# Kernel optimization log

Measured on AMD Instinct MI355X. Metric: run time of the kernel, lower is better.

## Reference

```python
import jax, jax.numpy as jnp
import numpy as np

B, S, D, DFF, H, V, L = 2, 1024, 1024, 4096, 16, 32000, 8
DH = D // H
EPS = 1e-5

def _pe():
    pos = np.arange(S, dtype=np.float32)[:, None]
    div = np.exp(np.arange(0, D, 2, dtype=np.float32) * (-np.log(10000.0) / D))
    pe = np.zeros((S, D), dtype=np.float32)
    pe[:, 0::2] = np.sin(pos * div)
    pe[:, 1::2] = np.cos(pos * div)
    return jnp.asarray(pe)

PE = _pe()

def _ln(h, g, b):
    m = jnp.mean(h, axis=-1, keepdims=True)
    v = jnp.mean((h - m) ** 2, axis=-1, keepdims=True)
    return (h - m) * jax.lax.rsqrt(v + EPS) * g + b

def setup_inputs():
    key = jax.random.key(0)
    k = jax.random.split(key, 16)
    sc = 0.02
    return {
        'x': jax.random.randint(k[0], (B, S), 0, V),
        'mask': jnp.tril(jnp.ones((1, 1, S, S), dtype=bool)),
        'emb': jax.random.normal(k[1], (V, D)) * sc,
        'Wq': jax.random.normal(k[2], (L, D, D)) * sc,
        'Wk': jax.random.normal(k[3], (L, D, D)) * sc,
        'Wv': jax.random.normal(k[4], (L, D, D)) * sc,
        'Wo': jax.random.normal(k[5], (L, D, D)) * sc,
        'ln1_g': jnp.ones((L, D)), 'ln1_b': jnp.zeros((L, D)),
        'ln2_g': jnp.ones((L, D)), 'ln2_b': jnp.zeros((L, D)),
        'W1': jax.random.normal(k[6], (L, D, DFF)) * sc,
        'b1': jnp.zeros((L, DFF)),
        'W2': jax.random.normal(k[7], (L, DFF, D)) * sc,
        'b2': jnp.zeros((L, D)),
        'lnf_g': jnp.ones((D,)), 'lnf_b': jnp.zeros((D,)),
        'projW': jax.random.normal(k[8], (D, V)) * sc,
        'projb': jnp.zeros((V,)),
    }

def reference(x, mask, emb, Wq, Wk, Wv, Wo, ln1_g, ln1_b, ln2_g, ln2_b,
              W1, b1, W2, b2, lnf_g, lnf_b, projW, projb):
    # embedding * sqrt(D) + positional encoding
    h = emb[x] * jnp.sqrt(jnp.float32(D)) + PE[None, :, :]
    scale = 1.0 / jnp.sqrt(jnp.float32(DH))
    for i in range(L):
        # --- self-attention sublayer (pre-LN residual) ---
        a_in = _ln(h, ln1_g[i], ln1_b[i])
        q = (a_in @ Wq[i]).reshape(B, S, H, DH)
        kk = (a_in @ Wk[i]).reshape(B, S, H, DH)
        v = (a_in @ Wv[i]).reshape(B, S, H, DH)
        scores = jnp.einsum('bqhd,bkhd->bhqk', q, kk) * scale
        scores = jnp.where(mask, scores, -1e9)
        attn = jax.nn.softmax(scores, axis=-1)
        o = jnp.einsum('bhqk,bkhd->bqhd', attn, v).reshape(B, S, D)
        h = h + o @ Wo[i]
        # --- feed-forward sublayer ---
        f_in = _ln(h, ln2_g[i], ln2_b[i])
        h = h + (jax.nn.relu(f_in @ W1[i] + b1[i]) @ W2[i] + b2[i])
    h = _ln(h, lnf_g, lnf_b)
    return h @ projW + projb
```

## Files before the change

### kernel.cpp

```cpp
#include <hip/hip_runtime.h>

typedef __bf16 bf16;
typedef __bf16 bf16x4 __attribute__((ext_vector_type(4)));
typedef __bf16 bf16x8 __attribute__((ext_vector_type(8)));
typedef float f32x4 __attribute__((ext_vector_type(4)));
typedef short short4v __attribute__((ext_vector_type(4)));

__device__ __forceinline__ short f2bs(float x) {
  bf16 hv = (bf16)x;
  return __builtin_bit_cast(short, hv);
}

__device__ __forceinline__ void gl_lds16(const void* g, void* l) {
  __builtin_amdgcn_global_load_lds(
      (const __attribute__((address_space(1))) unsigned int*)g,
      (__attribute__((address_space(3))) unsigned int*)l, 16, 0, 0);
}

__global__ __launch_bounds__(256) void wt_k(const float* __restrict__ in,
    bf16* __restrict__ out, int K, int N, long in_ls, long out_ls)
{
  __shared__ float t[64][33];
  const int z = blockIdx.z;
  const float* ip = in + (size_t)z * in_ls;
  bf16* op = out + (size_t)z * out_ls;
  const int n0 = blockIdx.x * 32, k0 = blockIdx.y * 64;
  const int tid = threadIdx.x;
  const int kr = tid >> 3, nc = (tid & 7) * 4;
#pragma unroll
  for (int hh = 0; hh < 2; ++hh) {
    float4 v = *(const float4*)(ip + (size_t)(k0 + kr + hh * 32) * N + n0 + nc);
    t[kr + hh * 32][nc]     = v.x;
    t[kr + hh * 32][nc + 1] = v.y;
    t[kr + hh * 32][nc + 2] = v.z;
    t[kr + hh * 32][nc + 3] = v.w;
  }
  __syncthreads();
  const int nr = tid >> 3, kc = (tid & 7) * 8;
  bf16x8 o;
#pragma unroll
  for (int j = 0; j < 8; ++j) o[j] = (bf16)t[kc + j][nr];
  *(bf16x8*)(op + (size_t)(n0 + nr) * K + k0 + kc) = o;
}

__global__ __launch_bounds__(256) void wt4_k(const float* __restrict__ Wq,
    const float* __restrict__ Wk, const float* __restrict__ Wv,
    const float* __restrict__ Wo, bf16* __restrict__ Bqkv,
    bf16* __restrict__ Bo)
{
  __shared__ float t[64][33];
  const int z = blockIdx.z;
  const int which = z >> 3, layer = z & 7;
  const long M1 = 1024 * 1024, M3 = 3 * M1;
  const float* ip = (which == 0 ? Wq : which == 1 ? Wk : which == 2 ? Wv : Wo)
                    + (size_t)layer * M1;
  bf16* op = (which < 3) ? (Bqkv + (size_t)layer * M3 + (size_t)which * M1)
                         : (Bo + (size_t)layer * M1);
  const int n0 = blockIdx.x * 32, k0 = blockIdx.y * 64;
  const int tid = threadIdx.x;
  const int kr = tid >> 3, nc = (tid & 7) * 4;
#pragma unroll
  for (int hh = 0; hh < 2; ++hh) {
    float4 v = *(const float4*)(ip + (size_t)(k0 + kr + hh * 32) * 1024 + n0 + nc);
    t[kr + hh * 32][nc]     = v.x;
    t[kr + hh * 32][nc + 1] = v.y;
    t[kr + hh * 32][nc + 2] = v.z;
    t[kr + hh * 32][nc + 3] = v.w;
  }
  __syncthreads();
  const int nr = tid >> 3, kc = (tid & 7) * 8;
  bf16x8 o;
#pragma unroll
  for (int j = 0; j < 8; ++j) o[j] = (bf16)t[kc + j][nr];
  *(bf16x8*)(op + (size_t)(n0 + nr) * 1024 + k0 + kc) = o;
}

__global__ __launch_bounds__(256) void embed_k(const int* __restrict__ x,
    const float* __restrict__ emb, float* __restrict__ h)
{
  const int m = blockIdx.x, t = threadIdx.x;
  const int s = m & 1023;
  const int tok = x[m];
  const int d0 = t * 4;
  float4 e = *(const float4*)(emb + (size_t)tok * 1024 + d0);
  const float* ep = &e.x;
  float r[4];
#pragma unroll
  for (int j = 0; j < 4; ++j) {
    int d = d0 + j;
    float freq = expf((float)(d & ~1) * (-9.2103403719761836f / 1024.f));
    float ang = (float)s * freq;
    float pe = (d & 1) ? cosf(ang) : sinf(ang);
    r[j] = ep[j] * 32.f + pe;
  }
  *(float4*)(h + (size_t)m * 1024 + d0) = make_float4(r[0], r[1], r[2], r[3]);
}

__global__ __launch_bounds__(256) void ln_k(const float* __restrict__ h,
    const float* __restrict__ g, const float* __restrict__ b,
    bf16* __restrict__ out)
{
  const int row = blockIdx.x, t = threadIdx.x;
  const float* hr = h + (size_t)row * 1024;
  float4 x = *(const float4*)(hr + t * 4);
  float s  = x.x + x.y + x.z + x.w;
  float ss = x.x * x.x + x.y * x.y + x.z * x.z + x.w * x.w;
#pragma unroll
  for (int off = 32; off >= 1; off >>= 1) {
    s  += __shfl_down(s, off);
    ss += __shfl_down(ss, off);
  }
  __shared__ float sb[4], ssb[4];
  if ((t & 63) == 0) { sb[t >> 6] = s; ssb[t >> 6] = ss; }
  __syncthreads();
  s  = sb[0] + sb[1] + sb[2] + sb[3];
  ss = ssb[0] + ssb[1] + ssb[2] + ssb[3];
  const float mean = s * (1.f / 1024.f);
  const float var  = ss * (1.f / 1024.f) - mean * mean;
  const float rstd = rsqrtf(var + 1e-5f);
  const float* xp = &x.x;
#pragma unroll
  for (int j = 0; j < 4; ++j) {
    int d = t * 4 + j;
    out[(size_t)row * 1024 + d] = (bf16)((xp[j] - mean) * rstd * g[d] + b[d]);
  }
}

__global__ __launch_bounds__(1024) void gemm256_k(
    const bf16* __restrict__ A, const bf16* __restrict__ Bt,
    const float* __restrict__ bias, float* __restrict__ C,
    int M, int N, int K)
{
  __shared__ __align__(16) bf16 As[2][256 * 64];
  __shared__ __align__(16) bf16 Bs[2][256 * 64];

  const int nwg = gridDim.x;
  const int orig = blockIdx.x;
  const int q8 = nwg >> 3, r8 = nwg & 7;
  const int xcd = orig & 7, loc = orig >> 3;
  const int wg = (xcd < r8 ? xcd * (q8 + 1) : r8 * (q8 + 1) + (xcd - r8) * q8) + loc;
  const int nrowt = M >> 8;
  const int rowt = wg & (nrowt - 1);
  const int colt = wg / nrowt;
  const int m0 = rowt * 256;
  const int n0 = colt * 256;
  const int nt = K >> 6;

  const int tid = threadIdx.x;
  const int lane = tid & 63;
  const int wbase = tid & ~63;
  const int wid = tid >> 6;
  const int wm = wid >> 2, wn = wid & 3;
  const int qr = lane & 15, grp = lane >> 4;

  f32x4 acc[4][4];
#pragma unroll
  for (int i = 0; i < 4; ++i)
#pragma unroll
    for (int j = 0; j < 4; ++j) acc[i][j] = (f32x4){0.f, 0.f, 0.f, 0.f};

  auto stage = [&](int bufi, int kt) {
#pragma unroll
    for (int it = 0; it < 2; ++it) {
      const int idx = it * 1024 + tid;
      const int row = idx >> 3, c = idx & 7;
      const int bo = (c * 16) ^ ((row & 7) << 4);
      gl_lds16((const char*)(A + (size_t)(m0 + row) * K + kt) + bo,
               (char*)&As[bufi][0] + (size_t)(it * 1024 + wbase) * 16);
    }
#pragma unroll
    for (int it = 0; it < 2; ++it) {
      const int idx = it * 1024 + tid;
      const int row = idx >> 3, c = idx & 7;
      const int bo = (c * 16) ^ ((row & 7) << 4);
      gl_lds16((const char*)(Bt + (size_t)(n0 + row) * K + kt) + bo,
               (char*)&Bs[bufi][0] + (size_t)(it * 1024 + wbase) * 16);
    }
  };

  stage(0, 0);
  for (int t = 0; t < nt; ++t) {
    const int cur = t & 1;
    if (t + 1 < nt) {
      stage(cur ^ 1, (t + 1) * 64);
      asm volatile("s_waitcnt vmcnt(4)" ::: "memory");
    } else {
      asm volatile("s_waitcnt vmcnt(0)" ::: "memory");
    }
    __builtin_amdgcn_s_barrier();
    asm volatile("" ::: "memory");
#pragma unroll
    for (int ks = 0; ks < 2; ++ks) {
      bf16x8 af[4], bfr[4];
#pragma unroll
      for (int mi = 0; mi < 4; ++mi) {
        const int arow = wm * 64 + mi * 16 + qr;
        const int ab = arow * 128 + ((grp * 16 + ks * 64) ^ ((arow & 7) << 4));
        af[mi] = *(const bf16x8*)((const char*)&As[cur][0] + ab);
      }
#pragma unroll
      for (int ni = 0; ni < 4; ++ni) {
        const int brow = wn * 64 + ni * 16 + qr;
        const int bb = brow * 128 + ((grp * 16 + ks * 64) ^ ((brow & 7) << 4));
        bfr[ni] = *(const bf16x8*)((const char*)&Bs[cur][0] + bb);
      }
      __builtin_amdgcn_s_setprio(1);
#pragma unroll
      for (int mi = 0; mi < 4; ++mi)
#pragma unroll
        for (int ni = 0; ni < 4; ++ni)
          acc[mi][ni] = __builtin_amdgcn_mfma_f32_16x16x32_bf16(
              bfr[ni], af[mi], acc[mi][ni], 0, 0, 0);
      __builtin_amdgcn_s_setprio(0);
    }
    __builtin_amdgcn_s_barrier();
    asm volatile("" ::: "memory");
  }

#pragma unroll
  for (int mi = 0; mi < 4; ++mi) {
    const int rowg = m0 + wm * 64 + mi * 16 + qr;
#pragma unroll
    for (int ni = 0; ni < 4; ++ni) {
      const int colg = n0 + wn * 64 + ni * 16 + grp * 4;
      float4 bv = *(const float4*)(bias + colg);
      float4 o;
      o.x = acc[mi][ni][0] + bv.x;
      o.y = acc[mi][ni][1] + bv.y;
      o.z = acc[mi][ni][2] + bv.z;
      o.w = acc[mi][ni][3] + bv.w;
      *(float4*)(C + (size_t)rowg * N + colg) = o;
    }
  }
}

template<int MODE, int NSPLIT>
__global__ __launch_bounds__(512) void gemm8_k(
    const bf16* __restrict__ A, const bf16* __restrict__ Bt,
    const float* __restrict__ bias, void* __restrict__ Cout,
    float* __restrict__ Hacc, bf16* __restrict__ Vt,
    int M, int N, int K)
{
  __shared__ __align__(16) bf16 As[2][128 * 64];
  __shared__ __align__(16) bf16 Bs[2][128 * 64];

  const int nwg = gridDim.x;
  const int orig = blockIdx.x;
  const int q8 = nwg >> 3, r8 = nwg & 7;
  const int xcd = orig & 7, loc = orig >> 3;
  const int wg = (xcd < r8 ? xcd * (q8 + 1) : r8 * (q8 + 1) + (xcd - r8) * q8) + loc;
  const int nrowt = M >> 7;
  const int ntiles = nrowt * (N >> 7);
  const int split = (NSPLIT > 1) ? (wg / ntiles) : 0;
  const int tile  = (NSPLIT > 1) ? (wg % ntiles) : wg;
  const int rowt = tile & (nrowt - 1);
  const int colt = tile / nrowt;
  const int m0 = rowt * 128;
  const int n0 = colt * 128;
  const int Ks = K / NSPLIT;
  const int k_begin = split * Ks;
  const int nt = Ks >> 6;

  const int tid = threadIdx.x;
  const int lane = tid & 63;
  const int wbase = tid & ~63;
  const int wid = tid >> 6;
  const int wm = wid >> 2;
  const int wn = wid & 3;
  const int qr = lane & 15, grp = lane >> 4;

  f32x4 acc[4][2];
#pragma unroll
  for (int i = 0; i < 4; ++i)
#pragma unroll
    for (int j = 0; j < 2; ++j) acc[i][j] = (f32x4){0.f, 0.f, 0.f, 0.f};

  auto stage = [&](int bufi, int kt) {
#pragma unroll
    for (int it = 0; it < 2; ++it) {
      const int idx = it * 512 + tid;
      const int row = idx >> 3, c = idx & 7;
      const int bo = (c * 16) ^ ((row & 7) << 4);
      gl_lds16((const char*)(A + (size_t)(m0 + row) * K + kt) + bo,
               (char*)&As[bufi][0] + (size_t)(it * 512 + wbase) * 16);
    }
#pragma unroll
    for (int it = 0; it < 2; ++it) {
      const int idx = it * 512 + tid;
      const int row = idx >> 3, c = idx & 7;
      const int bo = (c * 16) ^ ((row & 7) << 4);
      gl_lds16((const char*)(Bt + (size_t)(n0 + row) * K + kt) + bo,
               (char*)&Bs[bufi][0] + (size_t)(it * 512 + wbase) * 16);
    }
  };

  stage(0, k_begin);
  for (int t = 0; t < nt; ++t) {
    const int cur = t & 1;
    if (t + 1 < nt) {
      stage(cur ^ 1, k_begin + (t + 1) * 64);
      asm volatile("s_waitcnt vmcnt(4)" ::: "memory");
    } else {
      asm volatile("s_waitcnt vmcnt(0)" ::: "memory");
    }
    __builtin_amdgcn_s_barrier();
    asm volatile("" ::: "memory");
#pragma unroll
    for (int ks = 0; ks < 2; ++ks) {
      bf16x8 af[4], bfr[2];
#pragma unroll
      for (int mi = 0; mi < 4; ++mi) {
        const int arow = wm * 64 + mi * 16 + qr;
        const int ab = arow * 128 + ((grp * 16 + ks * 64) ^ ((arow & 7) << 4));
        af[mi] = *(const bf16x8*)((const char*)&As[cur][0] + ab);
      }
#pragma unroll
      for (int ni = 0; ni < 2; ++ni) {
        const int brow = wn * 32 + ni * 16 + qr;
        const int bb = brow * 128 + ((grp * 16 + ks * 64) ^ ((brow & 7) << 4));
        bfr[ni] = *(const bf16x8*)((const char*)&Bs[cur][0] + bb);
      }
      __builtin_amdgcn_s_setprio(1);
#pragma unroll
      for (int mi = 0; mi < 4; ++mi)
#pragma unroll
        for (int ni = 0; ni < 2; ++ni)
          acc[mi][ni] = __builtin_amdgcn_mfma_f32_16x16x32_bf16(
              af[mi], bfr[ni], acc[mi][ni], 0, 0, 0);
      __builtin_amdgcn_s_setprio(0);
    }
    __builtin_amdgcn_s_barrier();
    asm volatile("" ::: "memory");
  }

  const int sel = (MODE == 5) ? (n0 >> 10) : 0;
#pragma unroll
  for (int ni = 0; ni < 2; ++ni) {
    const int coln = wn * 32 + ni * 16 + qr;
    const int colg = n0 + coln;
    float bv = 0.f;
    if (MODE == 1) bv = bias[colg];
    if (MODE == 3 && split == 0) bv = bias[colg];
#pragma unroll
    for (int mi = 0; mi < 4; ++mi) {
      const int rowg0 = m0 + wm * 64 + mi * 16 + grp * 4;
      if (MODE == 5 && sel == 2) {
        const int b = rowg0 >> 10, s = rowg0 & 1023;
        bf16x4 pv;
#pragma unroll
        for (int r = 0; r < 4; ++r) pv[r] = (bf16)acc[mi][ni][r];
        *(bf16x4*)(Vt + (size_t)b * 1024 * 1024 + (size_t)(colg & 1023) * 1024 + s) = pv;
      } else {
#pragma unroll
        for (int r = 0; r < 4; ++r) {
          const int rowg = rowg0 + r;
          float v = acc[mi][ni][r];
          if (MODE == 1) {
            v += bv; v = v > 0.f ? v : 0.f;
            ((bf16*)Cout)[(size_t)rowg * N + colg] = (bf16)v;
          } else if (MODE == 2) {
            if (NSPLIT > 1) atomicAdd(&Hacc[(size_t)rowg * N + colg], v);
            else            Hacc[(size_t)rowg * N + colg] += v;
          } else if (MODE == 3) {
            if (NSPLIT > 1) atomicAdd(&Hacc[(size_t)rowg * N + colg], v + bv);
            else            Hacc[(size_t)rowg * N + colg] += v + bv;
          } else if (MODE == 5) {
            bf16* cb = (bf16*)Cout + (size_t)sel * 2048 * 1024;
            cb[(size_t)rowg * 1024 + (colg & 1023)] = (bf16)v;
          }
        }
      }
    }
  }
}

__global__ __launch_bounds__(64) void attn_k(const bf16* __restrict__ qm,
    const bf16* __restrict__ km, const bf16* __restrict__ vt,
    bf16* __restrict__ om)
{
  const int lane = threadIdx.x;
  const int qr = lane & 15, g = lane >> 4;
  const int qt = blockIdx.x & 63;
  const int hh = (blockIdx.x >> 6) & 15;
  const int bb = blockIdx.x >> 10;
  const size_t rowb = (size_t)bb * 1024;
  const int hb = hh * 64;

  const bf16* qp = qm + (rowb + qt * 16 + qr) * 1024 + hb + g * 8;
  const bf16x8 qf0 = *(const bf16x8*)qp;
  const bf16x8 qf1 = *(const bf16x8*)(qp + 32);

  const float SC = 0.125f * 1.4426950408889634f;

  float m_run = -1e30f, l_run = 0.f;
  f32x4 oacc[4];
#pragma unroll
  for (int dt = 0; dt < 4; ++dt) oacc[dt] = (f32x4){0.f, 0.f, 0.f, 0.f};

  const int qglob = qt * 16 + qr;
  const bf16* vtb = vt + (size_t)bb * 1024 * 1024;
  const bf16* kbase = km + rowb * 1024 + hb;

  auto tile_step = [&](int kvt, bool masked) {
    const bf16* kp = kbase + (size_t)kvt * 16 * 1024 + qr * 1024 + g * 8;
    bf16x8 kf0 = *(const bf16x8*)kp;
    bf16x8 kf1 = *(const bf16x8*)(kp + 32);
    bf16x4 vf[4];
#pragma unroll
    for (int dt = 0; dt < 4; ++dt)
      vf[dt] = *(const bf16x4*)(vtb + (size_t)(hb + dt * 16 + qr) * 1024 + kvt * 16 + g * 4);
    f32x4 st = (f32x4){0.f, 0.f, 0.f, 0.f};
    st = __builtin_amdgcn_mfma_f32_16x16x32_bf16(kf0, qf0, st, 0, 0, 0);
    st = __builtin_amdgcn_mfma_f32_16x16x32_bf16(kf1, qf1, st, 0, 0, 0);
    float sc[4];
#pragma unroll
    for (int r = 0; r < 4; ++r) {
      sc[r] = st[r] * SC;
      if (masked && (kvt * 16 + g * 4 + r > qglob)) sc[r] = -1e30f;
    }
    float mloc = fmaxf(fmaxf(sc[0], sc[1]), fmaxf(sc[2], sc[3]));
    mloc = fmaxf(mloc, __shfl_xor(mloc, 16));
    mloc = fmaxf(mloc, __shfl_xor(mloc, 32));
    float m_new = fmaxf(m_run, mloc);
    float alpha = exp2f(m_run - m_new);
    float p[4], ps = 0.f;
#pragma unroll
    for (int r = 0; r < 4; ++r) { p[r] = exp2f(sc[r] - m_new); ps += p[r]; }
    ps += __shfl_xor(ps, 16);
    ps += __shfl_xor(ps, 32);
    l_run = l_run * alpha + ps;
    m_run = m_new;
    short4v pfa;
#pragma unroll
    for (int r = 0; r < 4; ++r) pfa[r] = f2bs(p[r]);
#pragma unroll
    for (int dt = 0; dt < 4; ++dt) {
      oacc[dt] *= alpha;
      oacc[dt] = __builtin_amdgcn_mfma_f32_16x16x16bf16_1k(
          __builtin_bit_cast(short4v, vf[dt]), pfa, oacc[dt], 0, 0, 0);
    }
  };

  const int nun = qt;
  int kvt = 0;
  for (; kvt + 3 < nun; kvt += 4) {
    bf16x8 kf[4][2];
#pragma unroll
    for (int tt = 0; tt < 4; ++tt) {
      const bf16* kp = kbase + (size_t)(kvt + tt) * 16 * 1024 + qr * 1024 + g * 8;
      kf[tt][0] = *(const bf16x8*)kp;
      kf[tt][1] = *(const bf16x8*)(kp + 32);
    }
    bf16x4 vf[4][4];
#pragma unroll
    for (int tt = 0; tt < 4; ++tt)
#pragma unroll
      for (int dt = 0; dt < 4; ++dt)
        vf[tt][dt] = *(const bf16x4*)(vtb + (size_t)(hb + dt * 16 + qr) * 1024
                                      + (kvt + tt) * 16 + g * 4);
    f32x4 st[4];
#pragma unroll
    for (int tt = 0; tt < 4; ++tt) {
      st[tt] = (f32x4){0.f, 0.f, 0.f, 0.f};
      st[tt] = __builtin_amdgcn_mfma_f32_16x16x32_bf16(kf[tt][0], qf0, st[tt], 0, 0, 0);
      st[tt] = __builtin_amdgcn_mfma_f32_16x16x32_bf16(kf[tt][1], qf1, st[tt], 0, 0, 0);
    }
    float p[4][4];
    float mloc = -1e30f;
#pragma unroll
    for (int tt = 0; tt < 4; ++tt)
#pragma unroll
      for (int r = 0; r < 4; ++r) {
        p[tt][r] = st[tt][r] * SC;
        mloc = fmaxf(mloc, p[tt][r]);
      }
    mloc = fmaxf(mloc, __shfl_xor(mloc, 16));
    mloc = fmaxf(mloc, __shfl_xor(mloc, 32));
    if (!__all(mloc <= m_run + 8.f)) {
      float m_new = fmaxf(m_run, mloc);
      float alpha = exp2f(m_run - m_new);
      l_run *= alpha;
#pragma unroll
      for (int dt = 0; dt < 4; ++dt) oacc[dt] *= alpha;
      m_run = m_new;
    }
    float ps = 0.f;
#pragma unroll
    for (int tt = 0; tt < 4; ++tt)
#pragma unroll
      for (int r = 0; r < 4; ++r) {
        p[tt][r] = exp2f(p[tt][r] - m_run);
        ps += p[tt][r];
      }
    ps += __shfl_xor(ps, 16);
    ps += __shfl_xor(ps, 32);
    l_run += ps;
    short4v pf[4];
#pragma unroll
    for (int tt = 0; tt < 4; ++tt)
#pragma unroll
      for (int r = 0; r < 4; ++r) pf[tt][r] = f2bs(p[tt][r]);
#pragma unroll
    for (int dt = 0; dt < 4; ++dt)
#pragma unroll
      for (int tt = 0; tt < 4; ++tt)
        oacc[dt] = __builtin_amdgcn_mfma_f32_16x16x16bf16_1k(
            __builtin_bit_cast(short4v, vf[tt][dt]), pf[tt], oacc[dt], 0, 0, 0);
  }
  for (; kvt < nun; ++kvt) tile_step(kvt, false);
  tile_step(qt, true);

  const float inv = 1.f / l_run;
  bf16* op = om + (rowb + qt * 16 + qr) * 1024 + hb;
#pragma unroll
  for (int dt = 0; dt < 4; ++dt)
#pragma unroll
    for (int r = 0; r < 4; ++r)
      op[dt * 16 + g * 4 + r] = (bf16)(oacc[dt][r] * inv);
}

extern "C" void kernel_launch(void* const* d_in, const int* in_sizes, int n_in,
                              void* d_out, int out_size, void* d_ws, size_t ws_size,
                              hipStream_t stream)
{
  (void)in_sizes; (void)n_in; (void)out_size; (void)ws_size;
  const int*   x     = (const int*)d_in[0];
  const float* emb   = (const float*)d_in[2];
  const float* Wq    = (const float*)d_in[3];
  const float* Wk    = (const float*)d_in[4];
  const float* Wv    = (const float*)d_in[5];
  const float* Wo    = (const float*)d_in[6];
  const float* ln1g  = (const float*)d_in[7];
  const float* ln1b  = (const float*)d_in[8];
  const float* ln2g  = (const float*)d_in[9];
  const float* ln2b  = (const float*)d_in[10];
  const float* W1    = (const float*)d_in[11];
  const float* b1    = (const float*)d_in[12];
  const float* W2    = (const float*)d_in[13];
  const float* b2    = (const float*)d_in[14];
  const float* lnfg  = (const float*)d_in[15];
  const float* lnfb  = (const float*)d_in[16];
  const float* projW = (const float*)d_in[17];
  const float* projb = (const float*)d_in[18];

  char* ws = (char*)d_ws;
  const size_t MB = 1u << 20;
  float* h    = (float*)(ws + 0);
  bf16*  ain  = (bf16*)(ws + 8 * MB);
  bf16*  qb   = (bf16*)(ws + 12 * MB);
  bf16*  kb   = (bf16*)(ws + 16 * MB);
  bf16*  vtb  = (bf16*)(ws + 20 * MB);
  bf16*  ob   = (bf16*)(ws + 24 * MB);
  bf16*  mid  = (bf16*)(ws + 28 * MB);
  bf16*  Bqkv = (bf16*)(ws + 44 * MB);
  bf16*  Bo   = (bf16*)(ws + 92 * MB);
  bf16*  B1t  = (bf16*)(ws + 108 * MB);
  bf16*  B2t  = (bf16*)(ws + 172 * MB);
  bf16*  Bprj = (bf16*)(ws + 236 * MB);

  const long M1 = 1024 * 1024, M3 = 3 * M1, M4 = 4 * M1;

  wt4_k<<<dim3(32, 16, 32),  256, 0, stream>>>(Wq, Wk, Wv, Wo, Bqkv, Bo);
  wt_k<<<dim3(128, 16, 8),   256, 0, stream>>>(W1, B1t,     1024, 4096, M4, M4);
  wt_k<<<dim3(32, 64, 8),    256, 0, stream>>>(W2, B2t,     4096, 1024, M4, M4);
  wt_k<<<dim3(1000, 16, 1),  256, 0, stream>>>(projW, Bprj, 1024, 32000, 0, 0);

  embed_k<<<dim3(2048), 256, 0, stream>>>(x, emb, h);
  for (int i = 0; i < 8; ++i) {
    ln_k<<<dim3(2048), 256, 0, stream>>>(h, ln1g + i * 1024, ln1b + i * 1024, ain);
    gemm8_k<5,1><<<dim3(384), 512, 0, stream>>>(ain, Bqkv + i * M3, nullptr,
                                                qb, nullptr, vtb, 2048, 3072, 1024);
    attn_k<<<dim3(2048), 64, 0, stream>>>(qb, kb, vtb, ob);
    gemm8_k<2,2><<<dim3(256), 512, 0, stream>>>(ob, Bo + i * M1, nullptr,
                                                nullptr, h, nullptr, 2048, 1024, 1024);
    ln_k<<<dim3(2048), 256, 0, stream>>>(h, ln2g + i * 1024, ln2b + i * 1024, ain);
    gemm8_k<1,1><<<dim3(512), 512, 0, stream>>>(ain, B1t + i * M4, b1 + i * 4096,
                                                mid, nullptr, nullptr, 2048, 4096, 1024);
    gemm8_k<3,2><<<dim3(256), 512, 0, stream>>>(mid, B2t + i * M4, b2 + i * 1024,
                                                nullptr, h, nullptr, 2048, 1024, 4096);
  }
  ln_k<<<dim3(2048), 256, 0, stream>>>(h, lnfg, lnfb, ain);
  gemm256_k<<<dim3(1000), 1024, 0, stream>>>(ain, Bprj, projb,
                                             (float*)d_out, 2048, 32000, 1024);
}
```

Baseline: 2.096 ms.

## Run projection GEMM with 512 threads and interleaved staging; raise split-K to four

The final vocabulary projection GEMM now uses 8 waves instead of 16. Each wave computes a 128x64 sub-tile, and the next K tile is staged in four quarter chunks spread across the MMA phases. This is meant to overlap global-to-LDS loads with MFMA work and to cut barrier cost per wave, at the price of more accumulator registers and more barriers per K step. The Wo and W2 GEMMs also go from split-K 2 to split-K 4 with twice the workgroups, to raise parallelism, which adds more atomic or partial accumulation traffic into h.

```diff
diff --git a/kernel.cpp b/kernel.cpp
--- a/kernel.cpp
+++ b/kernel.cpp
@@ -126,7 +126,7 @@
   }
 }
 
-__global__ __launch_bounds__(1024) void gemm256_k(
+__global__ __launch_bounds__(512) void gemm256p_k(
     const bf16* __restrict__ A, const bf16* __restrict__ Bt,
     const float* __restrict__ bias, float* __restrict__ C,
     int M, int N, int K)
@@ -150,76 +150,79 @@
   const int lane = tid & 63;
   const int wbase = tid & ~63;
   const int wid = tid >> 6;
-  const int wm = wid >> 2, wn = wid & 3;
+  const int wm = wid >> 2;
+  const int wn = wid & 3;
   const int qr = lane & 15, grp = lane >> 4;
 
-  f32x4 acc[4][4];
-#pragma unroll
-  for (int i = 0; i < 4; ++i)
+  f32x4 acc[8][4];
+#pragma unroll
+  for (int i = 0; i < 8; ++i)
 #pragma unroll
     for (int j = 0; j < 4; ++j) acc[i][j] = (f32x4){0.f, 0.f, 0.f, 0.f};
 
-  auto stage = [&](int bufi, int kt) {
+  auto stageQ = [&](int bufi, int kt, int q) {
+    const bf16* base = (q < 2) ? A : Bt;
+    const int r0 = (q & 1) * 128;
+    const int t0 = (q < 2) ? m0 : n0;
+    bf16* lds = (q < 2) ? &As[bufi][0] : &Bs[bufi][0];
 #pragma unroll
     for (int it = 0; it < 2; ++it) {
-      const int idx = it * 1024 + tid;
+      const int idx = it * 512 + tid;
       const int row = idx >> 3, c = idx & 7;
       const int bo = (c * 16) ^ ((row & 7) << 4);
-      gl_lds16((const char*)(A + (size_t)(m0 + row) * K + kt) + bo,
-               (char*)&As[bufi][0] + (size_t)(it * 1024 + wbase) * 16);
-    }
-#pragma unroll
-    for (int it = 0; it < 2; ++it) {
-      const int idx = it * 1024 + tid;
-      const int row = idx >> 3, c = idx & 7;
-      const int bo = (c * 16) ^ ((row & 7) << 4);
-      gl_lds16((const char*)(Bt + (size_t)(n0 + row) * K + kt) + bo,
-               (char*)&Bs[bufi][0] + (size_t)(it * 1024 + wbase) * 16);
+      gl_lds16((const char*)(base + (size_t)(t0 + r0 + row) * K + kt) + bo,
+               (char*)lds + (size_t)(r0 * 8 + it * 512 + wbase) * 16);
     }
   };
 
-  stage(0, 0);
+  stageQ(0, 0, 0); stageQ(0, 0, 1); stageQ(0, 0, 2); stageQ(0, 0, 3);
+
+  bf16x8 bfr[4];
   for (int t = 0; t < nt; ++t) {
     const int cur = t & 1;
-    if (t + 1 < nt) {
-      stage(cur ^ 1, (t + 1) * 64);
-      asm volatile("s_waitcnt vmcnt(4)" ::: "memory");
-    } else {
-      asm volatile("s_waitcnt vmcnt(0)" ::: "memory");
-    }
-    __builtin_amdgcn_s_barrier();
-    asm volatile("" ::: "memory");
-#pragma unroll
-    for (int ks = 0; ks < 2; ++ks) {
-      bf16x8 af[4], bfr[4];
-#pragma unroll
-      for (int mi = 0; mi < 4; ++mi) {
-        const int arow = wm * 64 + mi * 16 + qr;
+    const int kt1 = (t + 1) * 64;
+    const bool pf = (t + 1 < nt);
+#pragma unroll
+    for (int p = 0; p < 4; ++p) {
+      if (pf) stageQ(cur ^ 1, kt1, p);
+      if (p == 0) {
+        if (pf) asm volatile("s_waitcnt vmcnt(2)" ::: "memory");
+        else    asm volatile("s_waitcnt vmcnt(0)" ::: "memory");
+        __builtin_amdgcn_s_barrier();
+        asm volatile("" ::: "memory");
+      }
+      const int ks = p >> 1, miq = p & 1;
+      bf16x8 af[4];
+#pragma unroll
+      for (int mi4 = 0; mi4 < 4; ++mi4) {
+        const int arow = wm * 128 + (miq * 4 + mi4) * 16 + qr;
         const int ab = arow * 128 + ((grp * 16 + ks * 64) ^ ((arow & 7) << 4));
-        af[mi] = *(const bf16x8*)((const char*)&As[cur][0] + ab);
-      }
-#pragma unroll
-      for (int ni = 0; ni < 4; ++ni) {
-        const int brow = wn * 64 + ni * 16 + qr;
-        const int bb = brow * 128 + ((grp * 16 + ks * 64) ^ ((brow & 7) << 4));
-        bfr[ni] = *(const bf16x8*)((const char*)&Bs[cur][0] + bb);
+        af[mi4] = *(const bf16x8*)((const char*)&As[cur][0] + ab);
+      }
+      if (miq == 0) {
+#pragma unroll
+        for (int ni = 0; ni < 4; ++ni) {
+          const int brow = wn * 64 + ni * 16 + qr;
+          const int bb = brow * 128 + ((grp * 16 + ks * 64) ^ ((brow & 7) << 4));
+          bfr[ni] = *(const bf16x8*)((const char*)&Bs[cur][0] + bb);
+        }
       }
       __builtin_amdgcn_s_setprio(1);
 #pragma unroll
-      for (int mi = 0; mi < 4; ++mi)
+      for (int mi4 = 0; mi4 < 4; ++mi4)
 #pragma unroll
         for (int ni = 0; ni < 4; ++ni)
-          acc[mi][ni] = __builtin_amdgcn_mfma_f32_16x16x32_bf16(
-              bfr[ni], af[mi], acc[mi][ni], 0, 0, 0);
+          acc[miq * 4 + mi4][ni] = __builtin_amdgcn_mfma_f32_16x16x32_bf16(
+              bfr[ni], af[mi4], acc[miq * 4 + mi4][ni], 0, 0, 0);
       __builtin_amdgcn_s_setprio(0);
-    }
-    __builtin_amdgcn_s_barrier();
-    asm volatile("" ::: "memory");
-  }
-
-#pragma unroll
-  for (int mi = 0; mi < 4; ++mi) {
-    const int rowg = m0 + wm * 64 + mi * 16 + qr;
+      __builtin_amdgcn_s_barrier();
+      asm volatile("" ::: "memory");
+    }
+  }
+
+#pragma unroll
+  for (int mi = 0; mi < 8; ++mi) {
+    const int rowg = m0 + wm * 128 + mi * 16 + qr;
 #pragma unroll
     for (int ni = 0; ni < 4; ++ni) {
       const int colg = n0 + wn * 64 + ni * 16 + grp * 4;
@@ -571,15 +574,15 @@
     gemm8_k<5,1><<<dim3(384), 512, 0, stream>>>(ain, Bqkv + i * M3, nullptr,
                                                 qb, nullptr, vtb, 2048, 3072, 1024);
     attn_k<<<dim3(2048), 64, 0, stream>>>(qb, kb, vtb, ob);
-    gemm8_k<2,2><<<dim3(256), 512, 0, stream>>>(ob, Bo + i * M1, nullptr,
+    gemm8_k<2,4><<<dim3(512), 512, 0, stream>>>(ob, Bo + i * M1, nullptr,
                                                 nullptr, h, nullptr, 2048, 1024, 1024);
     ln_k<<<dim3(2048), 256, 0, stream>>>(h, ln2g + i * 1024, ln2b + i * 1024, ain);
     gemm8_k<1,1><<<dim3(512), 512, 0, stream>>>(ain, B1t + i * M4, b1 + i * 4096,
                                                 mid, nullptr, nullptr, 2048, 4096, 1024);
-    gemm8_k<3,2><<<dim3(256), 512, 0, stream>>>(mid, B2t + i * M4, b2 + i * 1024,
+    gemm8_k<3,4><<<dim3(512), 512, 0, stream>>>(mid, B2t + i * M4, b2 + i * 1024,
                                                 nullptr, h, nullptr, 2048, 1024, 4096);
   }
   ln_k<<<dim3(2048), 256, 0, stream>>>(h, lnfg, lnfb, ain);
-  gemm256_k<<<dim3(1000), 1024, 0, stream>>>(ain, Bprj, projb,
+  gemm256p_k<<<dim3(1000), 512, 0, stream>>>(ain, Bprj, projb,
                                              (float*)d_out, 2048, 32000, 1024);
 }
```

Result: slower. 2.168 ms (+3.4%).
